# Kernel optimization log

Hardware: AMD Instinct MI355X
Metric: run time of the kernel (lower is better)

Reference implementation:

```python
import jax, jax.numpy as jnp
import numpy as np
import math

B, L, DIN, DOUT = 4, 1024, 64, 10
D, N = 512, 16            # hidden_dim (d_model), state_dim (d_state)
R = math.ceil(D / 16)     # dt_rank = 32
DT_MIN, DT_MAX = 1e-3, 1e-1


def _mamba_params(key):
    k1, k2, k3 = jax.random.split(key, 3)
    xproj_w = jax.random.normal(k1, (R + 2 * N, D), jnp.float32) * (D ** -0.5)
    dt_std = R ** -0.5
    dtproj_w = jax.random.uniform(k2, (D, R), jnp.float32, -dt_std, dt_std)
    dt = jnp.exp(jax.random.uniform(k3, (D,), jnp.float32)
                 * (math.log(DT_MAX) - math.log(DT_MIN)) + math.log(DT_MIN))
    dt = jnp.clip(dt, 1e-4, None)
    dtproj_b = dt + jnp.log(-jnp.expm1(-dt))          # inverse softplus
    A_log = jnp.log(jnp.broadcast_to(jnp.arange(1, N + 1, dtype=jnp.float32), (D, N)))
    Dp = jnp.ones((D,), jnp.float32)
    return xproj_w, dtproj_w, dtproj_b, A_log, Dp


def setup_inputs() -> dict:
    key = jax.random.key(0)
    ks = jax.random.split(key, 8)
    inp = {
        'x': jax.random.normal(ks[0], (B, L, DIN), jnp.float32),
        'W_in': jax.random.normal(ks[1], (D, DIN), jnp.float32) * (DIN ** -0.5),
        'b_in': jnp.zeros((D,), jnp.float32),
        'mix1_w': jax.random.normal(ks[2], (D, D), jnp.float32) * (D ** -0.5),
        'mix1_b': jnp.zeros((D,), jnp.float32),
        'mix2_w': jax.random.normal(ks[3], (D, D), jnp.float32) * (D ** -0.5),
        'mix2_b': jnp.zeros((D,), jnp.float32),
        'out_w': jax.random.normal(ks[4], (DOUT, D), jnp.float32) * (D ** -0.5),
        'out_b': jnp.zeros((DOUT,), jnp.float32),
    }
    (inp['m1_xproj'], inp['m1_dtw'], inp['m1_dtb'], inp['m1_Alog'], inp['m1_D']) = _mamba_params(ks[5])
    (inp['m2_xproj'], inp['m2_dtw'], inp['m2_dtb'], inp['m2_Alog'], inp['m2_D']) = _mamba_params(ks[6])
    return inp


def mamba_block(h, xproj_w, dtproj_w, dtproj_b, A_log, Dp):
    # h: (b, l, d) ; selective scan with A = -exp(A_log), delta_softplus=True
    b, l, d = h.shape
    A = -jnp.exp(A_log)                              # (d, n)
    x_dbl = jnp.einsum('bld,rd->blr', h, xproj_w)    # (b, l, r+2n)
    dt, Bm, Cm = jnp.split(x_dbl, [R, R + N], axis=-1)
    delta = jax.nn.softplus(jnp.einsum('blr,dr->bld', dt, dtproj_w) + dtproj_b)  # (b,l,d)
    dA = jnp.exp(delta[..., None] * A)                               # (b,l,d,n)
    dBu = delta[..., None] * Bm[:, :, None, :] * h[..., None]        # (b,l,d,n)

    def step(hstate, inp_t):
        dA_t, dBu_t, C_t = inp_t                     # (b,d,n),(b,d,n),(b,n)
        hstate = dA_t * hstate + dBu_t
        y = jnp.einsum('bdn,bn->bd', hstate, C_t)
        return hstate, y

    h0 = jnp.zeros((b, d, N), h.dtype)
    _, ys = jax.lax.scan(step, h0,
                         (jnp.swapaxes(dA, 0, 1), jnp.swapaxes(dBu, 0, 1), jnp.swapaxes(Cm, 0, 1)))
    y = jnp.swapaxes(ys, 0, 1) + h * Dp              # (b, l, d)
    return y


def reference(x, W_in, b_in, m1_xproj, m1_dtw, m1_dtb, m1_Alog, m1_D,
              mix1_w, mix1_b, m2_xproj, m2_dtw, m2_dtb, m2_Alog, m2_D,
              mix2_w, mix2_b, out_w, out_b):
    h = jnp.einsum('bli,di->bld', x, W_in) + b_in
    y = h
    h = mamba_block(h, m1_xproj, m1_dtw, m1_dtb, m1_Alog, m1_D)
    h = jax.nn.gelu(h, approximate=False)
    h = jnp.einsum('bld,ed->ble', h, mix1_w) + mix1_b
    h = h + y
    y = h
    h = mamba_block(h, m2_xproj, m2_dtw, m2_dtb, m2_Alog, m2_D)
    h = jax.nn.gelu(h, approximate=False)
    h = jnp.einsum('bld,ed->ble', h, mix2_w) + mix2_b
    h = h + y
    h = h.mean(axis=1)                               # (b, d)
    return jnp.einsum('bd,od->bo', h, out_w) + out_b
```

## Files before the change

kernel.cpp:

```cpp
#include <hip/hip_runtime.h>
#include <math.h>

typedef unsigned short ushort_t;
typedef short bf8_t __attribute__((ext_vector_type(8)));
typedef float f4_t  __attribute__((ext_vector_type(4)));

constexpr int B_   = 4;
constexpr int L_   = 1024;
constexpr int DIN_ = 64;
constexpr int DOUT_= 10;
constexpr int D_   = 512;
constexpr int N_   = 16;
constexpr int R_   = 32;
constexpr int RN_  = 64;
constexpr int M_   = B_ * L_;

constexpr int CN_ = 64;
constexpr int CL_ = L_ / CN_;

__device__ float    g_h   [M_ * D_];
__device__ float    g_h2  [M_ * D_];
__device__ ushort_t g_hbf [M_ * D_];
__device__ ushort_t g_gelubf[M_ * D_];
__device__ float    g_xdbl[M_ * RN_];
__device__ float2   g_dc  [M_ * D_];
__device__ float    g_stL  [B_ * CN_ * D_ * N_];
__device__ float    g_sumd [B_ * CN_ * D_];
__device__ float    g_carry[B_ * CN_ * D_ * N_];
__device__ float    g_mean [B_ * D_];
__device__ ushort_t g_w1bf [D_ * D_];
__device__ ushort_t g_w2bf [D_ * D_];
__device__ ushort_t g_xp1bf[RN_ * D_];
__device__ ushort_t g_xp2bf[RN_ * D_];

__device__ __forceinline__ float gelu_f(float x) {
  return 0.5f * x * (1.0f + erff(x * 0.7071067811865475f));
}
__device__ __forceinline__ float softplus_f(float x) {
  return fmaxf(x, 0.0f) + log1pf(__expf(-fabsf(x)));
}
__device__ __forceinline__ ushort_t f2bf(float x) {
  union { float f; unsigned u; } v; v.f = x;
  unsigned r = v.u + 0x7fffu + ((v.u >> 16) & 1u);
  return (ushort_t)(r >> 16);
}

__global__ __launch_bounds__(256) void k_cvt(const float* __restrict__ w1,
                                             const float* __restrict__ w2,
                                             const float* __restrict__ xp1,
                                             const float* __restrict__ xp2) {
  if (blockIdx.x == 576) {
#pragma unroll
    for (int j = 0; j < 8; ++j) g_mean[threadIdx.x * 8 + j] = 0.0f;
    return;
  }
  int i = (blockIdx.x * 256 + threadIdx.x) * 4;
  const float* src; ushort_t* dst; int off;
  if (i < 262144)      { src = w1;  dst = g_w1bf;  off = i; }
  else if (i < 524288) { src = w2;  dst = g_w2bf;  off = i - 262144; }
  else if (i < 557056) { src = xp1; dst = g_xp1bf; off = i - 524288; }
  else                 { src = xp2; dst = g_xp2bf; off = i - 557056; }
  float4 v = *(const float4*)&src[off];
  ushort4 o; o.x = f2bf(v.x); o.y = f2bf(v.y); o.z = f2bf(v.z); o.w = f2bf(v.w);
  *(ushort4*)&dst[off] = o;
}

template<int NN, int EPIM, bool DUAL, bool MEAN>
__device__ __forceinline__ void gemm_bf16_dev(
    const ushort_t* __restrict__ Abf, const ushort_t* __restrict__ Wbf,
    const float* __restrict__ bias, const float* __restrict__ res,
    float* __restrict__ out, ushort_t* __restrict__ obf) {
  __shared__ ushort_t As[64][72];
  __shared__ ushort_t Bs[64][72];
  constexpr int NB = NN / 64;
  const int tid  = threadIdx.x;
  const int m0   = (blockIdx.x / NB) * 64;
  const int n0   = (blockIdx.x % NB) * 64;
  const int lane = tid & 63;
  const int wv   = tid >> 6;
  const int quad = lane >> 4;
  const int ln   = lane & 15;
  const int mw   = (wv & 1) * 32;
  const int nw   = (wv >> 1) * 32;

  f4_t acc[2][2] = {};

  for (int k0 = 0; k0 < 512; k0 += 64) {
#pragma unroll
    for (int c = 0; c < 2; ++c) {
      int idx = tid + c * 256;
      int m = idx >> 3, kq = (idx & 7) << 3;
      *(float4*)&As[m][kq] = *(const float4*)&Abf[(size_t)(m0 + m) * 512 + k0 + kq];
      *(float4*)&Bs[m][kq] = *(const float4*)&Wbf[(size_t)(n0 + m) * 512 + k0 + kq];
    }
    __syncthreads();
#pragma unroll
    for (int k1 = 0; k1 < 64; k1 += 32) {
      bf8_t a0 = *(const bf8_t*)&As[mw +      ln][k1 + quad * 8];
      bf8_t a1 = *(const bf8_t*)&As[mw + 16 + ln][k1 + quad * 8];
      bf8_t b0 = *(const bf8_t*)&Bs[nw +      ln][k1 + quad * 8];
      bf8_t b1 = *(const bf8_t*)&Bs[nw + 16 + ln][k1 + quad * 8];
      acc[0][0] = __builtin_amdgcn_mfma_f32_16x16x32_bf16(a0, b0, acc[0][0], 0, 0, 0);
      acc[0][1] = __builtin_amdgcn_mfma_f32_16x16x32_bf16(a0, b1, acc[0][1], 0, 0, 0);
      acc[1][0] = __builtin_amdgcn_mfma_f32_16x16x32_bf16(a1, b0, acc[1][0], 0, 0, 0);
      acc[1][1] = __builtin_amdgcn_mfma_f32_16x16x32_bf16(a1, b1, acc[1][1], 0, 0, 0);
    }
    __syncthreads();
  }

  float bj[2] = {0.f, 0.f};
  if constexpr (EPIM == 1) {
    bj[0] = bias[n0 + nw + ln];
    bj[1] = bias[n0 + nw + 16 + ln];
  }
  float psum[2][2] = {{0.f, 0.f}, {0.f, 0.f}};
#pragma unroll
  for (int i = 0; i < 2; ++i)
#pragma unroll
    for (int j = 0; j < 2; ++j) {
      const int nc = n0 + nw + 16 * j + ln;
#pragma unroll
      for (int r = 0; r < 4; ++r) {
        const int row = m0 + mw + 16 * i + quad * 4 + r;
        const size_t idx = (size_t)row * NN + nc;
        float v = acc[i][j][r];
        if constexpr (EPIM == 1) v += bj[j] + res[idx];
        out[idx] = v;
        if constexpr (DUAL) obf[idx] = f2bf(v);
        if constexpr (MEAN) psum[i][j] += v;
      }
    }
  if constexpr (MEAN) {
    __shared__ float ssum[16][64];
#pragma unroll
    for (int i = 0; i < 2; ++i)
#pragma unroll
      for (int j = 0; j < 2; ++j) {
        const int rg = (wv & 1) * 8 + i * 4 + quad;
        const int cl = (wv >> 1) * 32 + j * 16 + ln;
        ssum[rg][cl] = psum[i][j];
      }
    __syncthreads();
    if (tid < 64) {
      float s = 0.f;
#pragma unroll
      for (int rg = 0; rg < 16; ++rg) s += ssum[rg][tid];
      const int b = m0 >> 10;
      atomicAdd(&g_mean[b * D_ + n0 + tid], s);
    }
  }
}

__global__ __launch_bounds__(256) void k_xdbl1g() {
  gemm_bf16_dev<64, 0, false, false>(g_hbf, g_xp1bf, nullptr, nullptr, g_xdbl, nullptr);
}
__global__ __launch_bounds__(256) void k_xdbl2g() {
  gemm_bf16_dev<64, 0, false, false>(g_hbf, g_xp2bf, nullptr, nullptr, g_xdbl, nullptr);
}
__global__ __launch_bounds__(256) void k_mix1g(const float* __restrict__ bias) {
  gemm_bf16_dev<512, 1, true, false>(g_gelubf, g_w1bf, bias, g_h, g_h2, g_hbf);
}
__global__ __launch_bounds__(256) void k_mix2g(const float* __restrict__ bias) {
  gemm_bf16_dev<512, 1, false, true>(g_gelubf, g_w2bf, bias, g_h2, g_h, nullptr);
}

__global__ __launch_bounds__(256) void k_in_mfma(const float* __restrict__ x,
                                                 const float* __restrict__ w,
                                                 const float* __restrict__ bias) {
  __shared__ ushort_t As[64][72];
  __shared__ ushort_t Bs[64][72];
  const int tid  = threadIdx.x;
  const int m0   = (blockIdx.x >> 3) * 64;
  const int n0   = (blockIdx.x & 7) * 64;
  const int lane = tid & 63;
  const int wv   = tid >> 6;
  const int quad = lane >> 4;
  const int ln   = lane & 15;
  const int mw   = (wv & 1) * 32;
  const int nw   = (wv >> 1) * 32;

  {
    const int m = tid >> 2, q = (tid & 3) << 4;
#pragma unroll
    for (int i = 0; i < 4; ++i) {
      float4 va = *(const float4*)&x[(size_t)(m0 + m) * 64 + q + i * 4];
      float4 vb = *(const float4*)&w[(size_t)(n0 + m) * 64 + q + i * 4];
      ushort4 oa, ob;
      oa.x = f2bf(va.x); oa.y = f2bf(va.y); oa.z = f2bf(va.z); oa.w = f2bf(va.w);
      ob.x = f2bf(vb.x); ob.y = f2bf(vb.y); ob.z = f2bf(vb.z); ob.w = f2bf(vb.w);
      *(ushort4*)&As[m][q + i * 4] = oa;
      *(ushort4*)&Bs[m][q + i * 4] = ob;
    }
  }
  __syncthreads();

  f4_t acc[2][2] = {};
#pragma unroll
  for (int k1 = 0; k1 < 64; k1 += 32) {
    bf8_t a0 = *(const bf8_t*)&As[mw +      ln][k1 + quad * 8];
    bf8_t a1 = *(const bf8_t*)&As[mw + 16 + ln][k1 + quad * 8];
    bf8_t b0 = *(const bf8_t*)&Bs[nw +      ln][k1 + quad * 8];
    bf8_t b1 = *(const bf8_t*)&Bs[nw + 16 + ln][k1 + quad * 8];
    acc[0][0] = __builtin_amdgcn_mfma_f32_16x16x32_bf16(a0, b0, acc[0][0], 0, 0, 0);
    acc[0][1] = __builtin_amdgcn_mfma_f32_16x16x32_bf16(a0, b1, acc[0][1], 0, 0, 0);
    acc[1][0] = __builtin_amdgcn_mfma_f32_16x16x32_bf16(a1, b0, acc[1][0], 0, 0, 0);
    acc[1][1] = __builtin_amdgcn_mfma_f32_16x16x32_bf16(a1, b1, acc[1][1], 0, 0, 0);
  }

  float bj[2] = { bias[n0 + nw + ln], bias[n0 + nw + 16 + ln] };
#pragma unroll
  for (int i = 0; i < 2; ++i)
#pragma unroll
    for (int j = 0; j < 2; ++j) {
      const int nc = n0 + nw + 16 * j + ln;
#pragma unroll
      for (int r = 0; r < 4; ++r) {
        const int row = m0 + mw + 16 * i + quad * 4 + r;
        const size_t idx = (size_t)row * D_ + nc;
        float v = acc[i][j][r] + bj[j];
        g_h[idx] = v;
        g_hbf[idx] = f2bf(v);
      }
    }
}

__device__ __forceinline__ void load_A(const float* __restrict__ Alog, int d,
                                       float* A) {
#pragma unroll
  for (int n = 0; n < 16; n += 4) {
    float4 t = *(const float4*)&Alog[d * N_ + n];
    A[n + 0] = -__expf(t.x); A[n + 1] = -__expf(t.y);
    A[n + 2] = -__expf(t.z); A[n + 3] = -__expf(t.w);
  }
}

__device__ __forceinline__ void dscan_p1_dev(const float* __restrict__ h,
                                             const float* __restrict__ dtw,
                                             const float* __restrict__ dtb,
                                             const float* __restrict__ Alog) {
  __shared__ float sdt[CL_][33];
  __shared__ float sB [CL_][16];
  const int d = threadIdx.x;
  const int c = blockIdx.x & (CN_ - 1);
  const int b = blockIdx.x / CN_;
  const int row0 = b * L_ + c * CL_;

  { int l = d >> 5, k = d & 31; sdt[l][k] = g_xdbl[(size_t)(row0 + l) * RN_ + k]; }
  if (d < CL_ * 16) {
    int l = d >> 4, n = d & 15;
    sB[l][n] = g_xdbl[(size_t)(row0 + l) * RN_ + R_ + n];
  }
  float w[32];
#pragma unroll
  for (int r = 0; r < 32; r += 4) {
    float4 t = *(const float4*)&dtw[d * R_ + r];
    w[r] = t.x; w[r + 1] = t.y; w[r + 2] = t.z; w[r + 3] = t.w;
  }
  const float bias = dtb[d];
  float A[16];
  load_A(Alog, d, A);
  __syncthreads();

  float st[16] = {};
  float sumd = 0.0f;
#pragma unroll
  for (int l = 0; l < CL_; ++l) {
    float acc = bias;
#pragma unroll
    for (int k = 0; k < 32; ++k) acc = fmaf(sdt[l][k], w[k], acc);
    const float delta = softplus_f(acc);
    const float hv = h[(size_t)(row0 + l) * D_ + d];
    const float dh = delta * hv;
    g_dc[(size_t)(row0 + l) * D_ + d] = make_float2(delta, dh);
    sumd += delta;
#pragma unroll
    for (int n = 0; n < 16; ++n) {
      float dA = __expf(delta * A[n]);
      st[n] = fmaf(dA, st[n], dh * sB[l][n]);
    }
  }
  const size_t o = ((size_t)(b * CN_ + c) * D_ + d) * N_;
#pragma unroll
  for (int n = 0; n < 16; n += 4)
    *(float4*)&g_stL[o + n] = make_float4(st[n], st[n+1], st[n+2], st[n+3]);
  g_sumd[(b * CN_ + c) * D_ + d] = sumd;
}

__global__ __launch_bounds__(512) void k_dscan1(const float* dtw, const float* dtb,
                                                const float* Alog) {
  dscan_p1_dev(g_h, dtw, dtb, Alog);
}
__global__ __launch_bounds__(512) void k_dscan2(const float* dtw, const float* dtb,
                                                const float* Alog) {
  dscan_p1_dev(g_h2, dtw, dtb, Alog);
}

__global__ __launch_bounds__(256) void k_scan_carry(const float* __restrict__ Alog) {
  const int g = blockIdx.x * 256 + threadIdx.x;
  const int n = g & 15;
  const int d = (g >> 4) & (D_ - 1);
  const int b = g >> 13;
  const float A = -__expf(Alog[d * N_ + n]);
  float carry = 0.0f;
#pragma unroll 4
  for (int c = 0; c < CN_; ++c) {
    const size_t idx = ((size_t)(b * CN_ + c) * D_ + d) * N_ + n;
    g_carry[idx] = carry;
    float P = __expf(A * g_sumd[(b * CN_ + c) * D_ + d]);
    carry = fmaf(P, carry, g_stL[idx]);
  }
}

__device__ __forceinline__ void scan_p2_dev(const float2* __restrict__ dc,
                                            const float*  __restrict__ xdbl,
                                            const float*  __restrict__ h,
                                            const float*  __restrict__ Alog,
                                            const float*  __restrict__ Dp,
                                            ushort_t* __restrict__ ybf) {
  __shared__ float sBC[CL_][32];
  const int d = threadIdx.x;
  const int c = blockIdx.x & (CN_ - 1);
  const int b = blockIdx.x / CN_;
  const int row0 = b * L_ + c * CL_;
  {
    int l = threadIdx.x >> 5, idx = threadIdx.x & 31;
    sBC[l][idx] = xdbl[(size_t)(row0 + l) * RN_ + R_ + idx];
  }
  float A[16];
  load_A(Alog, d, A);
  const float Dpv = Dp[d];
  __syncthreads();

  float st[16];
  const size_t o = ((size_t)(b * CN_ + c) * D_ + d) * N_;
#pragma unroll
  for (int n = 0; n < 16; n += 4) {
    float4 t = *(const float4*)&g_carry[o + n];
    st[n] = t.x; st[n+1] = t.y; st[n+2] = t.z; st[n+3] = t.w;
  }
#pragma unroll
  for (int l = 0; l < CL_; ++l) {
    float2 dcv = dc[(size_t)(row0 + l) * D_ + d];
    float y = 0.0f;
#pragma unroll
    for (int n = 0; n < 16; ++n) {
      float dA = __expf(dcv.x * A[n]);
      st[n] = fmaf(dA, st[n], dcv.y * sBC[l][n]);
      y = fmaf(st[n], sBC[l][16 + n], y);
    }
    float hv = h[(size_t)(row0 + l) * D_ + d];
    ybf[(size_t)(row0 + l) * D_ + d] = f2bf(gelu_f(y + hv * Dpv));
  }
}

__global__ __launch_bounds__(512) void k_scan1_p2(const float* Alog, const float* Dp) {
  scan_p2_dev(g_dc, g_xdbl, g_h, Alog, Dp, g_gelubf);
}
__global__ __launch_bounds__(512) void k_scan2_p2(const float* Alog, const float* Dp) {
  scan_p2_dev(g_dc, g_xdbl, g_h2, Alog, Dp, g_gelubf);
}

__global__ __launch_bounds__(512) void k_finalB(const float* out_w, const float* out_b,
                                                float* out) {
  __shared__ float sm[D_];
  __shared__ float sp[DOUT_ * 16];
  const int b = blockIdx.x, tid = threadIdx.x;
  sm[tid] = g_mean[b * D_ + tid] * (1.0f / L_);
  __syncthreads();
  if (tid < DOUT_ * 16) {
    int o = tid >> 4, seg = tid & 15;
    float p = 0.0f;
#pragma unroll
    for (int i = 0; i < 32; ++i)
      p += sm[seg * 32 + i] * out_w[o * D_ + seg * 32 + i];
    sp[tid] = p;
  }
  __syncthreads();
  if (tid < DOUT_) {
    float v = out_b[tid];
#pragma unroll
    for (int i = 0; i < 16; ++i) v += sp[tid * 16 + i];
    out[b * DOUT_ + tid] = v;
  }
}

extern "C" void kernel_launch(void* const* d_in, const int* in_sizes, int n_in,
                              void* d_out, int out_size, void* d_ws, size_t ws_size,
                              hipStream_t stream) {
  const float* x        = (const float*)d_in[0];
  const float* W_in     = (const float*)d_in[1];
  const float* b_in     = (const float*)d_in[2];
  const float* mix1_w   = (const float*)d_in[3];
  const float* mix1_b   = (const float*)d_in[4];
  const float* mix2_w   = (const float*)d_in[5];
  const float* mix2_b   = (const float*)d_in[6];
  const float* out_w    = (const float*)d_in[7];
  const float* out_b    = (const float*)d_in[8];
  const float* m1_xproj = (const float*)d_in[9];
  const float* m1_dtw   = (const float*)d_in[10];
  const float* m1_dtb   = (const float*)d_in[11];
  const float* m1_Alog  = (const float*)d_in[12];
  const float* m1_D     = (const float*)d_in[13];
  const float* m2_xproj = (const float*)d_in[14];
  const float* m2_dtw   = (const float*)d_in[15];
  const float* m2_dtb   = (const float*)d_in[16];
  const float* m2_Alog  = (const float*)d_in[17];
  const float* m2_D     = (const float*)d_in[18];
  float* out = (float*)d_out;

  const int gScan  = B_ * CN_;
  const int gCarry = (B_ * D_ * N_) / 256;
  const int gMix   = (M_ / 64) * (D_ / 64);
  const int gXdbl  = (M_ / 64);

  k_cvt    <<<577,  256, 0, stream>>>(mix1_w, mix2_w, m1_xproj, m2_xproj);
  k_in_mfma<<<gMix, 256, 0, stream>>>(x, W_in, b_in);

  k_xdbl1g  <<<gXdbl, 256, 0, stream>>>();
  k_dscan1  <<<gScan, 512, 0, stream>>>(m1_dtw, m1_dtb, m1_Alog);
  k_scan_carry<<<gCarry, 256, 0, stream>>>(m1_Alog);
  k_scan1_p2<<<gScan, 512, 0, stream>>>(m1_Alog, m1_D);
  k_mix1g   <<<gMix,  256, 0, stream>>>(mix1_b);
  k_xdbl2g  <<<gXdbl, 256, 0, stream>>>();
  k_dscan2  <<<gScan, 512, 0, stream>>>(m2_dtw, m2_dtb, m2_Alog);
  k_scan_carry<<<gCarry, 256, 0, stream>>>(m2_Alog);
  k_scan2_p2<<<gScan, 512, 0, stream>>>(m2_Alog, m2_D);
  k_mix2g   <<<gMix,  256, 0, stream>>>(mix2_b);
  k_finalB<<<B_, 512, 0, stream>>>(out_w, out_b, out);
}
```

Baseline: 244.6 us.

## Fuse chunked scan phases into one cooperative kernel with grid syncs

Merges the three selective-scan phases (chunk-local scan, carry propagation, final scan with output) into a single cooperative kernel per Mamba layer, separated by grid.sync. Delta, delta*h and h stay in registers across phases, so the g_dc intermediate buffer and its global write/read round trip go away, along with two kernel launches per layer. The carry phase also batches its loads 16 at a time. In exchange it raises register pressure (three 16-element arrays per thread), and it relies on all 256 blocks of 512 threads being co-resident, which cooperative launch requires.

Result: slower. 644.5 us (+163.5%).

```diff
diff --git a/kernel.cpp b/kernel.cpp
--- a/kernel.cpp
+++ b/kernel.cpp
@@ -1,5 +1,8 @@
 #include <hip/hip_runtime.h>
+#include <hip/hip_cooperative_groups.h>
 #include <math.h>
+
+namespace cg = cooperative_groups;
 
 typedef unsigned short ushort_t;
 typedef short bf8_t __attribute__((ext_vector_type(8)));
@@ -23,7 +26,6 @@
 __device__ ushort_t g_hbf [M_ * D_];
 __device__ ushort_t g_gelubf[M_ * D_];
 __device__ float    g_xdbl[M_ * RN_];
-__device__ float2   g_dc  [M_ * D_];
 __device__ float    g_stL  [B_ * CN_ * D_ * N_];
 __device__ float    g_sumd [B_ * CN_ * D_];
 __device__ float    g_carry[B_ * CN_ * D_ * N_];
@@ -234,130 +236,118 @@
   }
 }
 
-__device__ __forceinline__ void dscan_p1_dev(const float* __restrict__ h,
-                                             const float* __restrict__ dtw,
-                                             const float* __restrict__ dtb,
-                                             const float* __restrict__ Alog) {
+__device__ __forceinline__ void layer_dev(const float* __restrict__ h,
+                                          const float* __restrict__ dtw,
+                                          const float* __restrict__ dtb,
+                                          const float* __restrict__ Alog,
+                                          const float* __restrict__ Dp,
+                                          ushort_t* __restrict__ ybf) {
+  cg::grid_group grid = cg::this_grid();
   __shared__ float sdt[CL_][33];
-  __shared__ float sB [CL_][16];
-  const int d = threadIdx.x;
-  const int c = blockIdx.x & (CN_ - 1);
-  const int b = blockIdx.x / CN_;
-  const int row0 = b * L_ + c * CL_;
-
-  { int l = d >> 5, k = d & 31; sdt[l][k] = g_xdbl[(size_t)(row0 + l) * RN_ + k]; }
-  if (d < CL_ * 16) {
-    int l = d >> 4, n = d & 15;
-    sB[l][n] = g_xdbl[(size_t)(row0 + l) * RN_ + R_ + n];
-  }
-  float w[32];
-#pragma unroll
-  for (int r = 0; r < 32; r += 4) {
-    float4 t = *(const float4*)&dtw[d * R_ + r];
-    w[r] = t.x; w[r + 1] = t.y; w[r + 2] = t.z; w[r + 3] = t.w;
-  }
-  const float bias = dtb[d];
-  float A[16];
-  load_A(Alog, d, A);
-  __syncthreads();
-
-  float st[16] = {};
-  float sumd = 0.0f;
-#pragma unroll
-  for (int l = 0; l < CL_; ++l) {
-    float acc = bias;
-#pragma unroll
-    for (int k = 0; k < 32; ++k) acc = fmaf(sdt[l][k], w[k], acc);
-    const float delta = softplus_f(acc);
-    const float hv = h[(size_t)(row0 + l) * D_ + d];
-    const float dh = delta * hv;
-    g_dc[(size_t)(row0 + l) * D_ + d] = make_float2(delta, dh);
-    sumd += delta;
-#pragma unroll
-    for (int n = 0; n < 16; ++n) {
-      float dA = __expf(delta * A[n]);
-      st[n] = fmaf(dA, st[n], dh * sB[l][n]);
-    }
-  }
-  const size_t o = ((size_t)(b * CN_ + c) * D_ + d) * N_;
-#pragma unroll
-  for (int n = 0; n < 16; n += 4)
-    *(float4*)&g_stL[o + n] = make_float4(st[n], st[n+1], st[n+2], st[n+3]);
-  g_sumd[(b * CN_ + c) * D_ + d] = sumd;
-}
-
-__global__ __launch_bounds__(512) void k_dscan1(const float* dtw, const float* dtb,
-                                                const float* Alog) {
-  dscan_p1_dev(g_h, dtw, dtb, Alog);
-}
-__global__ __launch_bounds__(512) void k_dscan2(const float* dtw, const float* dtb,
-                                                const float* Alog) {
-  dscan_p1_dev(g_h2, dtw, dtb, Alog);
-}
-
-__global__ __launch_bounds__(256) void k_scan_carry(const float* __restrict__ Alog) {
-  const int g = blockIdx.x * 256 + threadIdx.x;
-  const int n = g & 15;
-  const int d = (g >> 4) & (D_ - 1);
-  const int b = g >> 13;
-  const float A = -__expf(Alog[d * N_ + n]);
-  float carry = 0.0f;
-#pragma unroll 4
-  for (int c = 0; c < CN_; ++c) {
-    const size_t idx = ((size_t)(b * CN_ + c) * D_ + d) * N_ + n;
-    g_carry[idx] = carry;
-    float P = __expf(A * g_sumd[(b * CN_ + c) * D_ + d]);
-    carry = fmaf(P, carry, g_stL[idx]);
-  }
-}
-
-__device__ __forceinline__ void scan_p2_dev(const float2* __restrict__ dc,
-                                            const float*  __restrict__ xdbl,
-                                            const float*  __restrict__ h,
-                                            const float*  __restrict__ Alog,
-                                            const float*  __restrict__ Dp,
-                                            ushort_t* __restrict__ ybf) {
   __shared__ float sBC[CL_][32];
   const int d = threadIdx.x;
   const int c = blockIdx.x & (CN_ - 1);
   const int b = blockIdx.x / CN_;
   const int row0 = b * L_ + c * CL_;
-  {
-    int l = threadIdx.x >> 5, idx = threadIdx.x & 31;
-    sBC[l][idx] = xdbl[(size_t)(row0 + l) * RN_ + R_ + idx];
-  }
+
+  { int l = d >> 5, k = d & 31; sdt[l][k] = g_xdbl[(size_t)(row0 + l) * RN_ + k]; }
+  { int l = d >> 5, k = d & 31; sBC[l][k] = g_xdbl[(size_t)(row0 + l) * RN_ + R_ + k]; }
+  float w[32];
+#pragma unroll
+  for (int r = 0; r < 32; r += 4) {
+    float4 t = *(const float4*)&dtw[d * R_ + r];
+    w[r] = t.x; w[r + 1] = t.y; w[r + 2] = t.z; w[r + 3] = t.w;
+  }
+  const float bias = dtb[d];
   float A[16];
   load_A(Alog, d, A);
   const float Dpv = Dp[d];
   __syncthreads();
 
-  float st[16];
-  const size_t o = ((size_t)(b * CN_ + c) * D_ + d) * N_;
-#pragma unroll
-  for (int n = 0; n < 16; n += 4) {
-    float4 t = *(const float4*)&g_carry[o + n];
-    st[n] = t.x; st[n+1] = t.y; st[n+2] = t.z; st[n+3] = t.w;
-  }
+  float delta[CL_], dh[CL_], hv[CL_];
+  float st[16] = {};
+  float sumd = 0.0f;
 #pragma unroll
   for (int l = 0; l < CL_; ++l) {
-    float2 dcv = dc[(size_t)(row0 + l) * D_ + d];
+    float acc = bias;
+#pragma unroll
+    for (int k = 0; k < 32; ++k) acc = fmaf(sdt[l][k], w[k], acc);
+    delta[l] = softplus_f(acc);
+    hv[l] = h[(size_t)(row0 + l) * D_ + d];
+    dh[l] = delta[l] * hv[l];
+    sumd += delta[l];
+#pragma unroll
+    for (int n = 0; n < 16; ++n) {
+      float dA = __expf(delta[l] * A[n]);
+      st[n] = fmaf(dA, st[n], dh[l] * sBC[l][n]);
+    }
+  }
+  {
+    const size_t o = ((size_t)(b * CN_ + c) * D_ + d) * N_;
+#pragma unroll
+    for (int n = 0; n < 16; n += 4)
+      *(float4*)&g_stL[o + n] = make_float4(st[n], st[n+1], st[n+2], st[n+3]);
+    g_sumd[(b * CN_ + c) * D_ + d] = sumd;
+  }
+  __threadfence();
+  grid.sync();
+
+  {
+    const int gid = blockIdx.x * 512 + threadIdx.x;
+    if (gid < B_ * D_ * N_) {
+      const int n  = gid & 15;
+      const int dd = (gid >> 4) & (D_ - 1);
+      const int bb = gid >> 13;
+      const float Ac = -__expf(Alog[dd * N_ + n]);
+      float carry = 0.0f;
+#pragma unroll
+      for (int c0 = 0; c0 < CN_; c0 += 16) {
+        float s[16], p[16];
+#pragma unroll
+        for (int j = 0; j < 16; ++j) {
+          const int cc = c0 + j;
+          s[j] = g_stL[((size_t)(bb * CN_ + cc) * D_ + dd) * N_ + n];
+          p[j] = g_sumd[(bb * CN_ + cc) * D_ + dd];
+        }
+#pragma unroll
+        for (int j = 0; j < 16; ++j) {
+          g_carry[((size_t)(bb * CN_ + c0 + j) * D_ + dd) * N_ + n] = carry;
+          carry = fmaf(__expf(Ac * p[j]), carry, s[j]);
+        }
+      }
+    }
+  }
+  __threadfence();
+  grid.sync();
+
+  {
+    const size_t o = ((size_t)(b * CN_ + c) * D_ + d) * N_;
+#pragma unroll
+    for (int n = 0; n < 16; n += 4) {
+      float4 t = *(const float4*)&g_carry[o + n];
+      st[n] = t.x; st[n+1] = t.y; st[n+2] = t.z; st[n+3] = t.w;
+    }
+  }
+#pragma unroll
+  for (int l = 0; l < CL_; ++l) {
     float y = 0.0f;
 #pragma unroll
     for (int n = 0; n < 16; ++n) {
-      float dA = __expf(dcv.x * A[n]);
-      st[n] = fmaf(dA, st[n], dcv.y * sBC[l][n]);
+      float dA = __expf(delta[l] * A[n]);
+      st[n] = fmaf(dA, st[n], dh[l] * sBC[l][n]);
       y = fmaf(st[n], sBC[l][16 + n], y);
     }
-    float hv = h[(size_t)(row0 + l) * D_ + d];
-    ybf[(size_t)(row0 + l) * D_ + d] = f2bf(gelu_f(y + hv * Dpv));
-  }
-}
-
-__global__ __launch_bounds__(512) void k_scan1_p2(const float* Alog, const float* Dp) {
-  scan_p2_dev(g_dc, g_xdbl, g_h, Alog, Dp, g_gelubf);
-}
-__global__ __launch_bounds__(512) void k_scan2_p2(const float* Alog, const float* Dp) {
-  scan_p2_dev(g_dc, g_xdbl, g_h2, Alog, Dp, g_gelubf);
+    ybf[(size_t)(row0 + l) * D_ + d] = f2bf(gelu_f(y + hv[l] * Dpv));
+  }
+}
+
+__global__ __launch_bounds__(512) void k_layer1(const float* dtw, const float* dtb,
+                                                const float* Alog, const float* Dp) {
+  layer_dev(g_h, dtw, dtb, Alog, Dp, g_gelubf);
+}
+__global__ __launch_bounds__(512) void k_layer2(const float* dtw, const float* dtb,
+                                                const float* Alog, const float* Dp) {
+  layer_dev(g_h2, dtw, dtb, Alog, Dp, g_gelubf);
 }
 
 __global__ __launch_bounds__(512) void k_finalB(const float* out_w, const float* out_b,
@@ -408,23 +398,24 @@
   const float* m2_D     = (const float*)d_in[18];
   float* out = (float*)d_out;
 
-  const int gScan  = B_ * CN_;
-  const int gCarry = (B_ * D_ * N_) / 256;
-  const int gMix   = (M_ / 64) * (D_ / 64);
-  const int gXdbl  = (M_ / 64);
+  const int gScan = B_ * CN_;
+  const int gMix  = (M_ / 64) * (D_ / 64);
+  const int gXdbl = (M_ / 64);
 
   k_cvt    <<<577,  256, 0, stream>>>(mix1_w, mix2_w, m1_xproj, m2_xproj);
   k_in_mfma<<<gMix, 256, 0, stream>>>(x, W_in, b_in);
 
-  k_xdbl1g  <<<gXdbl, 256, 0, stream>>>();
-  k_dscan1  <<<gScan, 512, 0, stream>>>(m1_dtw, m1_dtb, m1_Alog);
-  k_scan_carry<<<gCarry, 256, 0, stream>>>(m1_Alog);
-  k_scan1_p2<<<gScan, 512, 0, stream>>>(m1_Alog, m1_D);
-  k_mix1g   <<<gMix,  256, 0, stream>>>(mix1_b);
-  k_xdbl2g  <<<gXdbl, 256, 0, stream>>>();
-  k_dscan2  <<<gScan, 512, 0, stream>>>(m2_dtw, m2_dtb, m2_Alog);
-  k_scan_carry<<<gCarry, 256, 0, stream>>>(m2_Alog);
-  k_scan2_p2<<<gScan, 512, 0, stream>>>(m2_Alog, m2_D);
-  k_mix2g   <<<gMix,  256, 0, stream>>>(mix2_b);
+  k_xdbl1g<<<gXdbl, 256, 0, stream>>>();
+  {
+    void* args[] = { (void*)&m1_dtw, (void*)&m1_dtb, (void*)&m1_Alog, (void*)&m1_D };
+    hipLaunchCooperativeKernel((void*)k_layer1, dim3(gScan), dim3(512), args, 0, stream);
+  }
+  k_mix1g<<<gMix, 256, 0, stream>>>(mix1_b);
+  k_xdbl2g<<<gXdbl, 256, 0, stream>>>();
+  {
+    void* args[] = { (void*)&m2_dtw, (void*)&m2_dtb, (void*)&m2_Alog, (void*)&m2_D };
+    hipLaunchCooperativeKernel((void*)k_layer2, dim3(gScan), dim3(512), args, 0, stream);
+  }
+  k_mix2g<<<gMix, 256, 0, stream>>>(mix2_b);
   k_finalB<<<B_, 512, 0, stream>>>(out_w, out_b, out);
 }
```

## Recompute delta in scan pass 2 instead of storing it, and merge prologue kernels

Applied to the files above, without the earlier changes.

Drops the g_dc (delta, delta*h) buffer, which costs 16MB of writes and reads per Mamba block. Pass 2 of the scan now recomputes delta from dt_proj weights and the xdbl rows, trading extra FMA and softplus work for that traffic. The conversion kernel and the input-projection GEMM are merged into one launch, removing one kernel launch. The carry kernel batches its loads 16 chunks at a time so more memory requests are in flight.

Result: no change. 240.7 us (-1.6%).

```diff
diff --git a/kernel.cpp b/kernel.cpp
--- a/kernel.cpp
+++ b/kernel.cpp
@@ -23,7 +23,6 @@
 __device__ ushort_t g_hbf [M_ * D_];
 __device__ ushort_t g_gelubf[M_ * D_];
 __device__ float    g_xdbl[M_ * RN_];
-__device__ float2   g_dc  [M_ * D_];
 __device__ float    g_stL  [B_ * CN_ * D_ * N_];
 __device__ float    g_sumd [B_ * CN_ * D_];
 __device__ float    g_carry[B_ * CN_ * D_ * N_];
@@ -45,16 +44,82 @@
   return (ushort_t)(r >> 16);
 }
 
-__global__ __launch_bounds__(256) void k_cvt(const float* __restrict__ w1,
+__device__ __forceinline__ void in_mfma_part(int bx,
+                                             const float* __restrict__ x,
+                                             const float* __restrict__ w,
+                                             const float* __restrict__ bias) {
+  __shared__ ushort_t As[64][72];
+  __shared__ ushort_t Bs[64][72];
+  const int tid  = threadIdx.x;
+  const int m0   = (bx >> 3) * 64;
+  const int n0   = (bx & 7) * 64;
+  const int lane = tid & 63;
+  const int wv   = tid >> 6;
+  const int quad = lane >> 4;
+  const int ln   = lane & 15;
+  const int mw   = (wv & 1) * 32;
+  const int nw   = (wv >> 1) * 32;
+
+  {
+    const int m = tid >> 2, q = (tid & 3) << 4;
+#pragma unroll
+    for (int i = 0; i < 4; ++i) {
+      float4 va = *(const float4*)&x[(size_t)(m0 + m) * 64 + q + i * 4];
+      float4 vb = *(const float4*)&w[(size_t)(n0 + m) * 64 + q + i * 4];
+      ushort4 oa, ob;
+      oa.x = f2bf(va.x); oa.y = f2bf(va.y); oa.z = f2bf(va.z); oa.w = f2bf(va.w);
+      ob.x = f2bf(vb.x); ob.y = f2bf(vb.y); ob.z = f2bf(vb.z); ob.w = f2bf(vb.w);
+      *(ushort4*)&As[m][q + i * 4] = oa;
+      *(ushort4*)&Bs[m][q + i * 4] = ob;
+    }
+  }
+  __syncthreads();
+
+  f4_t acc[2][2] = {};
+#pragma unroll
+  for (int k1 = 0; k1 < 64; k1 += 32) {
+    bf8_t a0 = *(const bf8_t*)&As[mw +      ln][k1 + quad * 8];
+    bf8_t a1 = *(const bf8_t*)&As[mw + 16 + ln][k1 + quad * 8];
+    bf8_t b0 = *(const bf8_t*)&Bs[nw +      ln][k1 + quad * 8];
+    bf8_t b1 = *(const bf8_t*)&Bs[nw + 16 + ln][k1 + quad * 8];
+    acc[0][0] = __builtin_amdgcn_mfma_f32_16x16x32_bf16(a0, b0, acc[0][0], 0, 0, 0);
+    acc[0][1] = __builtin_amdgcn_mfma_f32_16x16x32_bf16(a0, b1, acc[0][1], 0, 0, 0);
+    acc[1][0] = __builtin_amdgcn_mfma_f32_16x16x32_bf16(a1, b0, acc[1][0], 0, 0, 0);
+    acc[1][1] = __builtin_amdgcn_mfma_f32_16x16x32_bf16(a1, b1, acc[1][1], 0, 0, 0);
+  }
+
+  float bj[2] = { bias[n0 + nw + ln], bias[n0 + nw + 16 + ln] };
+#pragma unroll
+  for (int i = 0; i < 2; ++i)
+#pragma unroll
+    for (int j = 0; j < 2; ++j) {
+      const int nc = n0 + nw + 16 * j + ln;
+#pragma unroll
+      for (int r = 0; r < 4; ++r) {
+        const int row = m0 + mw + 16 * i + quad * 4 + r;
+        const size_t idx = (size_t)row * D_ + nc;
+        float v = acc[i][j][r] + bj[j];
+        g_h[idx] = v;
+        g_hbf[idx] = f2bf(v);
+      }
+    }
+}
+
+__global__ __launch_bounds__(256) void k_pre(const float* __restrict__ x,
+                                             const float* __restrict__ w_in,
+                                             const float* __restrict__ b_in,
+                                             const float* __restrict__ w1,
                                              const float* __restrict__ w2,
                                              const float* __restrict__ xp1,
                                              const float* __restrict__ xp2) {
-  if (blockIdx.x == 576) {
+  const int bx = blockIdx.x;
+  if (bx < 512) { in_mfma_part(bx, x, w_in, b_in); return; }
+  if (bx == 1088) {
 #pragma unroll
     for (int j = 0; j < 8; ++j) g_mean[threadIdx.x * 8 + j] = 0.0f;
     return;
   }
-  int i = (blockIdx.x * 256 + threadIdx.x) * 4;
+  int i = ((bx - 512) * 256 + threadIdx.x) * 4;
   const float* src; ushort_t* dst; int off;
   if (i < 262144)      { src = w1;  dst = g_w1bf;  off = i; }
   else if (i < 524288) { src = w2;  dst = g_w2bf;  off = i - 262144; }
@@ -164,66 +229,6 @@
   gemm_bf16_dev<512, 1, false, true>(g_gelubf, g_w2bf, bias, g_h2, g_h, nullptr);
 }
 
-__global__ __launch_bounds__(256) void k_in_mfma(const float* __restrict__ x,
-                                                 const float* __restrict__ w,
-                                                 const float* __restrict__ bias) {
-  __shared__ ushort_t As[64][72];
-  __shared__ ushort_t Bs[64][72];
-  const int tid  = threadIdx.x;
-  const int m0   = (blockIdx.x >> 3) * 64;
-  const int n0   = (blockIdx.x & 7) * 64;
-  const int lane = tid & 63;
-  const int wv   = tid >> 6;
-  const int quad = lane >> 4;
-  const int ln   = lane & 15;
-  const int mw   = (wv & 1) * 32;
-  const int nw   = (wv >> 1) * 32;
-
-  {
-    const int m = tid >> 2, q = (tid & 3) << 4;
-#pragma unroll
-    for (int i = 0; i < 4; ++i) {
-      float4 va = *(const float4*)&x[(size_t)(m0 + m) * 64 + q + i * 4];
-      float4 vb = *(const float4*)&w[(size_t)(n0 + m) * 64 + q + i * 4];
-      ushort4 oa, ob;
-      oa.x = f2bf(va.x); oa.y = f2bf(va.y); oa.z = f2bf(va.z); oa.w = f2bf(va.w);
-      ob.x = f2bf(vb.x); ob.y = f2bf(vb.y); ob.z = f2bf(vb.z); ob.w = f2bf(vb.w);
-      *(ushort4*)&As[m][q + i * 4] = oa;
-      *(ushort4*)&Bs[m][q + i * 4] = ob;
-    }
-  }
-  __syncthreads();
-
-  f4_t acc[2][2] = {};
-#pragma unroll
-  for (int k1 = 0; k1 < 64; k1 += 32) {
-    bf8_t a0 = *(const bf8_t*)&As[mw +      ln][k1 + quad * 8];
-    bf8_t a1 = *(const bf8_t*)&As[mw + 16 + ln][k1 + quad * 8];
-    bf8_t b0 = *(const bf8_t*)&Bs[nw +      ln][k1 + quad * 8];
-    bf8_t b1 = *(const bf8_t*)&Bs[nw + 16 + ln][k1 + quad * 8];
-    acc[0][0] = __builtin_amdgcn_mfma_f32_16x16x32_bf16(a0, b0, acc[0][0], 0, 0, 0);
-    acc[0][1] = __builtin_amdgcn_mfma_f32_16x16x32_bf16(a0, b1, acc[0][1], 0, 0, 0);
-    acc[1][0] = __builtin_amdgcn_mfma_f32_16x16x32_bf16(a1, b0, acc[1][0], 0, 0, 0);
-    acc[1][1] = __builtin_amdgcn_mfma_f32_16x16x32_bf16(a1, b1, acc[1][1], 0, 0, 0);
-  }
-
-  float bj[2] = { bias[n0 + nw + ln], bias[n0 + nw + 16 + ln] };
-#pragma unroll
-  for (int i = 0; i < 2; ++i)
-#pragma unroll
-    for (int j = 0; j < 2; ++j) {
-      const int nc = n0 + nw + 16 * j + ln;
-#pragma unroll
-      for (int r = 0; r < 4; ++r) {
-        const int row = m0 + mw + 16 * i + quad * 4 + r;
-        const size_t idx = (size_t)row * D_ + nc;
-        float v = acc[i][j][r] + bj[j];
-        g_h[idx] = v;
-        g_hbf[idx] = f2bf(v);
-      }
-    }
-}
-
 __device__ __forceinline__ void load_A(const float* __restrict__ Alog, int d,
                                        float* A) {
 #pragma unroll
@@ -234,10 +239,10 @@
   }
 }
 
-__device__ __forceinline__ void dscan_p1_dev(const float* __restrict__ h,
-                                             const float* __restrict__ dtw,
-                                             const float* __restrict__ dtb,
-                                             const float* __restrict__ Alog) {
+__device__ __forceinline__ void scan_p1_dev(const float* __restrict__ h,
+                                            const float* __restrict__ dtw,
+                                            const float* __restrict__ dtb,
+                                            const float* __restrict__ Alog) {
   __shared__ float sdt[CL_][33];
   __shared__ float sB [CL_][16];
   const int d = threadIdx.x;
@@ -269,9 +274,7 @@
 #pragma unroll
     for (int k = 0; k < 32; ++k) acc = fmaf(sdt[l][k], w[k], acc);
     const float delta = softplus_f(acc);
-    const float hv = h[(size_t)(row0 + l) * D_ + d];
-    const float dh = delta * hv;
-    g_dc[(size_t)(row0 + l) * D_ + d] = make_float2(delta, dh);
+    const float dh = delta * h[(size_t)(row0 + l) * D_ + d];
     sumd += delta;
 #pragma unroll
     for (int n = 0; n < 16; ++n) {
@@ -286,13 +289,13 @@
   g_sumd[(b * CN_ + c) * D_ + d] = sumd;
 }
 
-__global__ __launch_bounds__(512) void k_dscan1(const float* dtw, const float* dtb,
-                                                const float* Alog) {
-  dscan_p1_dev(g_h, dtw, dtb, Alog);
-}
-__global__ __launch_bounds__(512) void k_dscan2(const float* dtw, const float* dtb,
-                                                const float* Alog) {
-  dscan_p1_dev(g_h2, dtw, dtb, Alog);
+__global__ __launch_bounds__(512) void k_p1_1(const float* dtw, const float* dtb,
+                                              const float* Alog) {
+  scan_p1_dev(g_h, dtw, dtb, Alog);
+}
+__global__ __launch_bounds__(512) void k_p1_2(const float* dtw, const float* dtb,
+                                              const float* Alog) {
+  scan_p1_dev(g_h2, dtw, dtb, Alog);
 }
 
 __global__ __launch_bounds__(256) void k_scan_carry(const float* __restrict__ Alog) {
@@ -302,30 +305,44 @@
   const int b = g >> 13;
   const float A = -__expf(Alog[d * N_ + n]);
   float carry = 0.0f;
-#pragma unroll 4
-  for (int c = 0; c < CN_; ++c) {
-    const size_t idx = ((size_t)(b * CN_ + c) * D_ + d) * N_ + n;
-    g_carry[idx] = carry;
-    float P = __expf(A * g_sumd[(b * CN_ + c) * D_ + d]);
-    carry = fmaf(P, carry, g_stL[idx]);
-  }
-}
-
-__device__ __forceinline__ void scan_p2_dev(const float2* __restrict__ dc,
-                                            const float*  __restrict__ xdbl,
-                                            const float*  __restrict__ h,
-                                            const float*  __restrict__ Alog,
-                                            const float*  __restrict__ Dp,
+#pragma unroll
+  for (int c0 = 0; c0 < CN_; c0 += 16) {
+    float s[16], p[16];
+#pragma unroll
+    for (int j = 0; j < 16; ++j) {
+      s[j] = g_stL[((size_t)(b * CN_ + c0 + j) * D_ + d) * N_ + n];
+      p[j] = g_sumd[(b * CN_ + c0 + j) * D_ + d];
+    }
+#pragma unroll
+    for (int j = 0; j < 16; ++j) {
+      g_carry[((size_t)(b * CN_ + c0 + j) * D_ + d) * N_ + n] = carry;
+      carry = fmaf(__expf(A * p[j]), carry, s[j]);
+    }
+  }
+}
+
+__device__ __forceinline__ void scan_p2_dev(const float* __restrict__ h,
+                                            const float* __restrict__ dtw,
+                                            const float* __restrict__ dtb,
+                                            const float* __restrict__ Alog,
+                                            const float* __restrict__ Dp,
                                             ushort_t* __restrict__ ybf) {
+  __shared__ float sdt[CL_][33];
   __shared__ float sBC[CL_][32];
   const int d = threadIdx.x;
   const int c = blockIdx.x & (CN_ - 1);
   const int b = blockIdx.x / CN_;
   const int row0 = b * L_ + c * CL_;
-  {
-    int l = threadIdx.x >> 5, idx = threadIdx.x & 31;
-    sBC[l][idx] = xdbl[(size_t)(row0 + l) * RN_ + R_ + idx];
-  }
+
+  { int l = d >> 5, k = d & 31; sdt[l][k] = g_xdbl[(size_t)(row0 + l) * RN_ + k]; }
+  { int l = d >> 5, k = d & 31; sBC[l][k] = g_xdbl[(size_t)(row0 + l) * RN_ + R_ + k]; }
+  float w[32];
+#pragma unroll
+  for (int r = 0; r < 32; r += 4) {
+    float4 t = *(const float4*)&dtw[d * R_ + r];
+    w[r] = t.x; w[r + 1] = t.y; w[r + 2] = t.z; w[r + 3] = t.w;
+  }
+  const float bias = dtb[d];
   float A[16];
   load_A(Alog, d, A);
   const float Dpv = Dp[d];
@@ -340,24 +357,30 @@
   }
 #pragma unroll
   for (int l = 0; l < CL_; ++l) {
-    float2 dcv = dc[(size_t)(row0 + l) * D_ + d];
+    float acc = bias;
+#pragma unroll
+    for (int k = 0; k < 32; ++k) acc = fmaf(sdt[l][k], w[k], acc);
+    const float delta = softplus_f(acc);
+    const float hv = h[(size_t)(row0 + l) * D_ + d];
+    const float dh = delta * hv;
     float y = 0.0f;
 #pragma unroll
     for (int n = 0; n < 16; ++n) {
-      float dA = __expf(dcv.x * A[n]);
-      st[n] = fmaf(dA, st[n], dcv.y * sBC[l][n]);
+      float dA = __expf(delta * A[n]);
+      st[n] = fmaf(dA, st[n], dh * sBC[l][n]);
       y = fmaf(st[n], sBC[l][16 + n], y);
     }
-    float hv = h[(size_t)(row0 + l) * D_ + d];
     ybf[(size_t)(row0 + l) * D_ + d] = f2bf(gelu_f(y + hv * Dpv));
   }
 }
 
-__global__ __launch_bounds__(512) void k_scan1_p2(const float* Alog, const float* Dp) {
-  scan_p2_dev(g_dc, g_xdbl, g_h, Alog, Dp, g_gelubf);
-}
-__global__ __launch_bounds__(512) void k_scan2_p2(const float* Alog, const float* Dp) {
-  scan_p2_dev(g_dc, g_xdbl, g_h2, Alog, Dp, g_gelubf);
+__global__ __launch_bounds__(512) void k_p2_1(const float* dtw, const float* dtb,
+                                              const float* Alog, const float* Dp) {
+  scan_p2_dev(g_h, dtw, dtb, Alog, Dp, g_gelubf);
+}
+__global__ __launch_bounds__(512) void k_p2_2(const float* dtw, const float* dtb,
+                                              const float* Alog, const float* Dp) {
+  scan_p2_dev(g_h2, dtw, dtb, Alog, Dp, g_gelubf);
 }
 
 __global__ __launch_bounds__(512) void k_finalB(const float* out_w, const float* out_b,
@@ -413,18 +436,17 @@
   const int gMix   = (M_ / 64) * (D_ / 64);
   const int gXdbl  = (M_ / 64);
 
-  k_cvt    <<<577,  256, 0, stream>>>(mix1_w, mix2_w, m1_xproj, m2_xproj);
-  k_in_mfma<<<gMix, 256, 0, stream>>>(x, W_in, b_in);
-
-  k_xdbl1g  <<<gXdbl, 256, 0, stream>>>();
-  k_dscan1  <<<gScan, 512, 0, stream>>>(m1_dtw, m1_dtb, m1_Alog);
+  k_pre<<<1089, 256, 0, stream>>>(x, W_in, b_in, mix1_w, mix2_w, m1_xproj, m2_xproj);
+
+  k_xdbl1g    <<<gXdbl,  256, 0, stream>>>();
+  k_p1_1      <<<gScan,  512, 0, stream>>>(m1_dtw, m1_dtb, m1_Alog);
   k_scan_carry<<<gCarry, 256, 0, stream>>>(m1_Alog);
-  k_scan1_p2<<<gScan, 512, 0, stream>>>(m1_Alog, m1_D);
-  k_mix1g   <<<gMix,  256, 0, stream>>>(mix1_b);
-  k_xdbl2g  <<<gXdbl, 256, 0, stream>>>();
-  k_dscan2  <<<gScan, 512, 0, stream>>>(m2_dtw, m2_dtb, m2_Alog);
+  k_p2_1      <<<gScan,  512, 0, stream>>>(m1_dtw, m1_dtb, m1_Alog, m1_D);
+  k_mix1g     <<<gMix,   256, 0, stream>>>(mix1_b);
+  k_xdbl2g    <<<gXdbl,  256, 0, stream>>>();
+  k_p1_2      <<<gScan,  512, 0, stream>>>(m2_dtw, m2_dtb, m2_Alog);
   k_scan_carry<<<gCarry, 256, 0, stream>>>(m2_Alog);
-  k_scan2_p2<<<gScan, 512, 0, stream>>>(m2_Alog, m2_D);
-  k_mix2g   <<<gMix,  256, 0, stream>>>(mix2_b);
+  k_p2_2      <<<gScan,  512, 0, stream>>>(m2_dtw, m2_dtb, m2_Alog, m2_D);
+  k_mix2g     <<<gMix,   256, 0, stream>>>(mix2_b);
   k_finalB<<<B_, 512, 0, stream>>>(out_w, out_b, out);
 }
```
